# Kernel optimization log

Hardware: AMD Instinct MI355X
Metric: run time of the kernel (lower is better)

## Reference

```python
import jax, jax.numpy as jnp
import numpy as np

K = 16                 # k nearest neighbors
POS_LO, POS_HI = 0, 3  # position_slice
INF = jnp.float32(1e30)


def setup_inputs() -> dict:
    key = jax.random.key(0)
    k1, k2, k3 = jax.random.split(key, 3)
    B, N, F = 16, 2048, 128
    nodes = jax.random.normal(k1, (B, N, F), dtype=jnp.float32)
    T = jax.random.randint(k2, (B,), 0, 1024)
    taus = jax.random.randint(k3, (B,), 0, 1024)
    return {"nodes": nodes, "T": T, "taus": taus, "B": B}


def reference(nodes, T, taus, B):
    # Faithful, vectorized version of the per-batch causal KNN edge builder.
    # Original: for each batch b, sinks = pos[b, T[b]:T[b]+taus[b]],
    # sources = pos[b, :T[b]+taus[b]]; knn(source, sink, k) returns
    # (sink_local_idx, source_idx); keep edges where sink_local > source;
    # assemble COO adjacency (b, sink_local, source) with weight 1.
    # Here we return the equivalent DENSE [B, N, N] adjacency.
    pos = nodes[:, :, POS_LO:POS_HI]              # [B, N, d]
    N = pos.shape[1]
    i_idx = jnp.arange(N)                         # local sink index grid
    # global index of sink i in batch b is T[b] + i
    sink_gidx = jnp.clip(T[:, None] + i_idx[None, :], 0, N - 1)   # [B, N]
    sink_pos = jnp.take_along_axis(pos, sink_gidx[..., None], axis=1)  # [B, N, d]
    sink_valid = i_idx[None, :] < taus[:, None]                    # [B, N]
    src_valid = i_idx[None, :] < (T + taus)[:, None]               # [B, N]
    # squared distances sink->source: [B, N_sink, N_src]
    d2 = jnp.sum((sink_pos[:, :, None, :] - pos[:, None, :, :]) ** 2, axis=-1)
    d2 = jnp.where(src_valid[:, None, :], d2, INF)
    neg_vals, nbr = jax.lax.top_k(-d2, K)          # k smallest distances, [B, N, K]
    nbr_valid = neg_vals > -INF                    # source actually existed
    causal = i_idx[None, :, None] > nbr            # edge[0] > edge[1] mask (local sink idx)
    valid = sink_valid[:, :, None] & nbr_valid & causal
    adj = jnp.zeros((B, N, N), dtype=jnp.float32)
    b_idx = jnp.arange(B)[:, None, None]
    adj = adj.at[b_idx, i_idx[None, :, None], nbr].add(
        jnp.where(valid, jnp.float32(1.0), jnp.float32(0.0)))
    return adj
```

## Files before the change

kernel.cpp:

```cpp
#include <hip/hip_runtime.h>

#define NN 2048
#define FF 128
#define KK 16

__global__ __launch_bounds__(256) void knn_adj_kernel(
    const float* __restrict__ nodes,
    const int*   __restrict__ T_arr,
    const int*   __restrict__ tau_arr,
    float*       __restrict__ adj)
{
    const int b   = blockIdx.x;
    const int i0  = blockIdx.y << 2;
    const int tid = threadIdx.x;
    const int wave = tid >> 6;
    const int lane = tid & 63;

    const int T   = T_arr[b];
    const int tau = tau_arr[b];

    float* block_out = adj + ((size_t)b * NN + i0) * NN;

    if (i0 >= tau) {
        float4 z = make_float4(0.f, 0.f, 0.f, 0.f);
        float4* out4 = (float4*)block_out;
        #pragma unroll
        for (int t = 0; t < 8; ++t)
            out4[tid + (t << 8)] = z;
        return;
    }

    const int M = T + tau;

    __shared__ float sx[NN], sy[NN], sz[NN];
    for (int j = tid; j < M; j += 256) {
        const float* p = nodes + ((size_t)b * NN + j) * FF;
        sx[j] = p[0];
        sy[j] = p[1];
        sz[j] = p[2];
    }
    __syncthreads();

    const int i = i0 + wave;
    float* row_out = block_out + (size_t)wave * NN;

    if (i >= tau) {
        float4 z = make_float4(0.f, 0.f, 0.f, 0.f);
        float4* out4 = (float4*)row_out;
        #pragma unroll
        for (int t = 0; t < 8; ++t)
            out4[lane + (t << 6)] = z;
        return;
    }

    const int g = T + i;
    const float sxv = sx[g], syv = sy[g], szv = sz[g];

    unsigned long long keys[32];
    #pragma unroll
    for (int s = 0; s < 32; ++s) {
        const int j = lane + (s << 6);
        unsigned long long key = ~0ull;
        if (j < M) {
            float dx = __fsub_rn(sxv, sx[j]);
            float dy = __fsub_rn(syv, sy[j]);
            float dz = __fsub_rn(szv, sz[j]);
            float d2 = __fadd_rn(__fadd_rn(__fmul_rn(dx, dx), __fmul_rn(dy, dy)),
                                 __fmul_rn(dz, dz));
            key = ((unsigned long long)__float_as_uint(d2) << 32)
                | (unsigned int)(j + 1);
        }
        keys[s] = key;
    }

    const unsigned long long INF_HI = (unsigned long long)__float_as_uint(1e30f);

    unsigned int colmask = 0;
    unsigned long long prev = 0;
    for (int k = 0; k < KK; ++k) {
        unsigned long long m = ~0ull;
        #pragma unroll
        for (int s = 0; s < 32; ++s) {
            unsigned long long key = keys[s];
            if (key > prev && key < m) m = key;
        }
        #pragma unroll
        for (int off = 32; off > 0; off >>= 1) {
            unsigned long long o = __shfl_xor(m, off, 64);
            if (o < m) m = o;
        }
        if ((m >> 32) >= INF_HI) break;
        prev = m;
        const int j = (int)(m & 0xffffffffu) - 1;
        if (j < i && ((j >> 2) & 63) == lane)
            colmask |= 1u << (((j >> 8) << 2) | (j & 3));
    }

    float4* out4 = (float4*)row_out;
    #pragma unroll
    for (int t = 0; t < 8; ++t) {
        float4 v;
        v.x = ((colmask >> (t * 4 + 0)) & 1u) ? 1.0f : 0.0f;
        v.y = ((colmask >> (t * 4 + 1)) & 1u) ? 1.0f : 0.0f;
        v.z = ((colmask >> (t * 4 + 2)) & 1u) ? 1.0f : 0.0f;
        v.w = ((colmask >> (t * 4 + 3)) & 1u) ? 1.0f : 0.0f;
        out4[(t << 6) + lane] = v;
    }
}

extern "C" void kernel_launch(void* const* d_in, const int* in_sizes, int n_in,
                              void* d_out, int out_size, void* d_ws, size_t ws_size,
                              hipStream_t stream) {
    const float* nodes = (const float*)d_in[0];
    const int*   T     = (const int*)d_in[1];
    const int*   taus  = (const int*)d_in[2];
    float*       adj   = (float*)d_out;

    const int B = in_sizes[1];
    dim3 grid(B, NN / 4);
    knn_adj_kernel<<<grid, dim3(256), 0, stream>>>(nodes, T, taus, adj);
}
```

Baseline: 319.9 us.

## Split KNN into bitmap kernel with per-lane top-4 queue plus separate adjacency writer

The KNN is split into two kernels when workspace allows. The first keeps a per-lane sorted queue of the 4 smallest keys, picks the winner with a 32-bit DPP wave-min on the distance only, and rescans just when a lane's queue empties. It writes a compact per-row bitmap. The second kernel expands that bitmap into the dense float adjacency with coalesced float4 stores. This removes the 32-slot register key array and the 16 full scans per row, and stores positions as float4 in shared memory. In exchange it adds a second launch, a round trip through the workspace bitmap, and a data-dependent rescan path.

```diff
diff --git a/kernel.cpp b/kernel.cpp
--- a/kernel.cpp
+++ b/kernel.cpp
@@ -3,8 +3,158 @@
 #define NN 2048
 #define FF 128
 #define KK 16
-
-__global__ __launch_bounds__(256) void knn_adj_kernel(
+#define INF_KEY 0xFFFFFFFFFFFFFFFFull
+
+__device__ __forceinline__ unsigned long long make_key(const float4& s,
+                                                       const float4& p, int j) {
+    float dx = __fsub_rn(s.x, p.x);
+    float dy = __fsub_rn(s.y, p.y);
+    float dz = __fsub_rn(s.z, p.z);
+    float d2 = __fadd_rn(__fadd_rn(__fmul_rn(dx, dx), __fmul_rn(dy, dy)),
+                         __fmul_rn(dz, dz));
+    return ((unsigned long long)__float_as_uint(d2) << 32) | (unsigned)(j + 1);
+}
+
+__device__ __forceinline__ unsigned wave_min_u32(unsigned x) {
+    int v = (int)x, t;
+    t = __builtin_amdgcn_update_dpp(v, v, 0x111, 0xf, 0xf, false);
+    v = ((unsigned)t < (unsigned)v) ? t : v;
+    t = __builtin_amdgcn_update_dpp(v, v, 0x112, 0xf, 0xf, false);
+    v = ((unsigned)t < (unsigned)v) ? t : v;
+    t = __builtin_amdgcn_update_dpp(v, v, 0x114, 0xf, 0xf, false);
+    v = ((unsigned)t < (unsigned)v) ? t : v;
+    t = __builtin_amdgcn_update_dpp(v, v, 0x118, 0xf, 0xf, false);
+    v = ((unsigned)t < (unsigned)v) ? t : v;
+    t = __builtin_amdgcn_update_dpp(v, v, 0x142, 0xf, 0xf, false);
+    v = ((unsigned)t < (unsigned)v) ? t : v;
+    t = __builtin_amdgcn_update_dpp(v, v, 0x143, 0xf, 0xf, false);
+    v = ((unsigned)t < (unsigned)v) ? t : v;
+    return (unsigned)__builtin_amdgcn_readlane(v, 63);
+}
+
+__global__ __launch_bounds__(256) void knn_bitmap_kernel(
+    const float* __restrict__ nodes,
+    const int*   __restrict__ T_arr,
+    const int*   __restrict__ tau_arr,
+    unsigned*    __restrict__ bm)
+{
+    const int b    = blockIdx.x;
+    const int i0   = blockIdx.y << 2;
+    const int tid  = threadIdx.x;
+    const int wave = tid >> 6;
+    const int lane = tid & 63;
+
+    const int tau = tau_arr[b];
+    if (i0 >= tau) return;
+    const int T = T_arr[b];
+    const int M = T + tau;
+
+    __shared__ float4 spos[NN];
+    for (int j = tid; j < M; j += 256)
+        spos[j] = *(const float4*)(nodes + ((size_t)b * NN + j) * FF);
+    __syncthreads();
+
+    const int i = i0 + wave;
+    if (i >= tau) return;
+
+    const float4 sp = spos[T + i];
+
+    unsigned long long q0 = INF_KEY, q1 = INF_KEY, q2 = INF_KEY, q3 = INF_KEY;
+    const int S = (M + 63) >> 6;
+    #pragma unroll 4
+    for (int s = 0; s < S; ++s) {
+        const int j = lane + (s << 6);
+        if (j < M) {
+            unsigned long long key = make_key(sp, spos[j], j);
+            if (key < q3) {
+                q3 = key;
+                unsigned long long t;
+                if (q3 < q2) { t = q2; q2 = q3; q3 = t; }
+                if (q2 < q1) { t = q1; q1 = q2; q2 = t; }
+                if (q1 < q0) { t = q0; q0 = q1; q1 = t; }
+            }
+        }
+    }
+
+    unsigned colmask = 0;
+    unsigned long long lastpop = 0;
+    for (int k = 0; k < KK; ++k) {
+        const unsigned hd = (unsigned)(q0 >> 32);
+        const unsigned m  = wave_min_u32(hd);
+        if (m == 0xFFFFFFFFu) break;
+
+        const unsigned long long mask = __ballot(hd == m);
+        unsigned jwin;
+        if (__popcll(mask) == 1) {
+            const int w = __builtin_ctzll(mask);
+            jwin = (unsigned)__builtin_amdgcn_readlane((int)(unsigned)q0, w);
+        } else {
+            unsigned jc = (hd == m) ? (unsigned)q0 : 0xFFFFFFFFu;
+            jwin = wave_min_u32(jc);
+        }
+        const int j = (int)jwin - 1;
+
+        if (j < i && (j >> 5) == lane)
+            colmask |= 1u << (j & 31);
+
+        if (hd == m && (unsigned)q0 == jwin) {
+            lastpop = ((unsigned long long)m << 32) | jwin;
+            q0 = q1; q1 = q2; q2 = q3; q3 = INF_KEY;
+            if (q0 == INF_KEY) {
+                unsigned long long best = INF_KEY;
+                for (int s2 = 0; s2 < S; ++s2) {
+                    const int jj = lane + (s2 << 6);
+                    if (jj < M) {
+                        unsigned long long kk = make_key(sp, spos[jj], jj);
+                        if (kk > lastpop && kk < best) best = kk;
+                    }
+                }
+                q0 = best;
+            }
+        }
+    }
+
+    bm[((size_t)b * NN + i) * 64 + lane] = colmask;
+}
+
+__global__ __launch_bounds__(256) void write_adj_kernel(
+    const unsigned* __restrict__ bm,
+    const int*      __restrict__ tau_arr,
+    float*          __restrict__ adj)
+{
+    const int b    = blockIdx.x;
+    const int i0   = blockIdx.y << 2;
+    const int tid  = threadIdx.x;
+    const int wave = tid >> 6;
+    const int lane = tid & 63;
+    const int i    = i0 + wave;
+    const int tau  = tau_arr[b];
+
+    float4* out4 = (float4*)(adj + ((size_t)b * NN + i) * NN);
+
+    if (i >= tau) {
+        const float4 z = make_float4(0.f, 0.f, 0.f, 0.f);
+        #pragma unroll
+        for (int k = 0; k < 8; ++k)
+            out4[(k << 6) + lane] = z;
+        return;
+    }
+
+    const unsigned* row = bm + ((size_t)b * NN + i) * 64;
+    #pragma unroll
+    for (int k = 0; k < 8; ++k) {
+        const unsigned w   = row[(k << 3) + (lane >> 3)];
+        const unsigned nib = (w >> ((lane & 7) << 2)) & 0xFu;
+        float4 v;
+        v.x = (nib & 1u) ? 1.0f : 0.0f;
+        v.y = (nib & 2u) ? 1.0f : 0.0f;
+        v.z = (nib & 4u) ? 1.0f : 0.0f;
+        v.w = (nib & 8u) ? 1.0f : 0.0f;
+        out4[(k << 6) + lane] = v;
+    }
+}
+
+__global__ __launch_bounds__(256) void knn_adj_fused(
     const float* __restrict__ nodes,
     const int*   __restrict__ T_arr,
     const int*   __restrict__ tau_arr,
@@ -15,47 +165,35 @@
     const int tid = threadIdx.x;
     const int wave = tid >> 6;
     const int lane = tid & 63;
-
     const int T   = T_arr[b];
     const int tau = tau_arr[b];
-
     float* block_out = adj + ((size_t)b * NN + i0) * NN;
 
     if (i0 >= tau) {
         float4 z = make_float4(0.f, 0.f, 0.f, 0.f);
         float4* out4 = (float4*)block_out;
         #pragma unroll
-        for (int t = 0; t < 8; ++t)
-            out4[tid + (t << 8)] = z;
+        for (int t = 0; t < 8; ++t) out4[tid + (t << 8)] = z;
         return;
     }
-
     const int M = T + tau;
-
     __shared__ float sx[NN], sy[NN], sz[NN];
     for (int j = tid; j < M; j += 256) {
         const float* p = nodes + ((size_t)b * NN + j) * FF;
-        sx[j] = p[0];
-        sy[j] = p[1];
-        sz[j] = p[2];
+        sx[j] = p[0]; sy[j] = p[1]; sz[j] = p[2];
     }
     __syncthreads();
-
     const int i = i0 + wave;
     float* row_out = block_out + (size_t)wave * NN;
-
     if (i >= tau) {
         float4 z = make_float4(0.f, 0.f, 0.f, 0.f);
         float4* out4 = (float4*)row_out;
         #pragma unroll
-        for (int t = 0; t < 8; ++t)
-            out4[lane + (t << 6)] = z;
+        for (int t = 0; t < 8; ++t) out4[lane + (t << 6)] = z;
         return;
     }
-
     const int g = T + i;
     const float sxv = sx[g], syv = sy[g], szv = sz[g];
-
     unsigned long long keys[32];
     #pragma unroll
     for (int s = 0; s < 32; ++s) {
@@ -67,15 +205,12 @@
             float dz = __fsub_rn(szv, sz[j]);
             float d2 = __fadd_rn(__fadd_rn(__fmul_rn(dx, dx), __fmul_rn(dy, dy)),
                                  __fmul_rn(dz, dz));
-            key = ((unsigned long long)__float_as_uint(d2) << 32)
-                | (unsigned int)(j + 1);
+            key = ((unsigned long long)__float_as_uint(d2) << 32) | (unsigned)(j + 1);
         }
         keys[s] = key;
     }
-
     const unsigned long long INF_HI = (unsigned long long)__float_as_uint(1e30f);
-
-    unsigned int colmask = 0;
+    unsigned colmask = 0;
     unsigned long long prev = 0;
     for (int k = 0; k < KK; ++k) {
         unsigned long long m = ~0ull;
@@ -95,7 +230,6 @@
         if (j < i && ((j >> 2) & 63) == lane)
             colmask |= 1u << (((j >> 8) << 2) | (j & 3));
     }
-
     float4* out4 = (float4*)row_out;
     #pragma unroll
     for (int t = 0; t < 8; ++t) {
@@ -115,8 +249,16 @@
     const int*   T     = (const int*)d_in[1];
     const int*   taus  = (const int*)d_in[2];
     float*       adj   = (float*)d_out;
-
     const int B = in_sizes[1];
-    dim3 grid(B, NN / 4);
-    knn_adj_kernel<<<grid, dim3(256), 0, stream>>>(nodes, T, taus, adj);
-}
+
+    const size_t bm_bytes = (size_t)B * NN * 64 * sizeof(unsigned);
+    if (ws_size >= bm_bytes) {
+        unsigned* bm = (unsigned*)d_ws;
+        dim3 grid(B, NN / 4);
+        knn_bitmap_kernel<<<grid, dim3(256), 0, stream>>>(nodes, T, taus, bm);
+        write_adj_kernel<<<grid, dim3(256), 0, stream>>>(bm, taus, adj);
+    } else {
+        dim3 grid(B, NN / 4);
+        knn_adj_fused<<<grid, dim3(256), 0, stream>>>(nodes, T, taus, adj);
+    }
+}
```

Measured after the change: 316.1 us. Within noise of the previous version (-1.2%).

## Replace 16-pass full rescan with per-lane top-4 queues and DPP wave min

Applied to the files above, without the earlier changes.

Each lane now keeps a sorted queue of its 4 smallest keys instead of 32 keys in registers. Neighbours are popped with a 32-bit DPP wave minimum on the distance, and ties are broken by a second reduction on the index. A lane whose queue empties recomputes distances to refill it. The output bitmask is changed to contiguous 32-column words and redistributed through shared memory so the stores can be written as float4. The goal is to drop the per-iteration scan over 32 registers and the 64-bit shuffle reduction, and to lower register pressure. The cost is occasional refill rescans when one lane holds more than 4 of the winners.

```diff
diff --git a/kernel.cpp b/kernel.cpp
--- a/kernel.cpp
+++ b/kernel.cpp
@@ -3,26 +3,42 @@
 #define NN 2048
 #define FF 128
 #define KK 16
+#define INF_KEY 0xFFFFFFFFFFFFFFFFull
 
-__global__ __launch_bounds__(256) void knn_adj_kernel(
+__device__ __forceinline__ unsigned wave_min_u32(unsigned x) {
+    int v = (int)x, t;
+    t = __builtin_amdgcn_update_dpp(v, v, 0x111, 0xf, 0xf, false);
+    v = ((unsigned)t < (unsigned)v) ? t : v;
+    t = __builtin_amdgcn_update_dpp(v, v, 0x112, 0xf, 0xf, false);
+    v = ((unsigned)t < (unsigned)v) ? t : v;
+    t = __builtin_amdgcn_update_dpp(v, v, 0x114, 0xf, 0xf, false);
+    v = ((unsigned)t < (unsigned)v) ? t : v;
+    t = __builtin_amdgcn_update_dpp(v, v, 0x118, 0xf, 0xf, false);
+    v = ((unsigned)t < (unsigned)v) ? t : v;
+    t = __builtin_amdgcn_update_dpp(v, v, 0x142, 0xf, 0xf, false);
+    v = ((unsigned)t < (unsigned)v) ? t : v;
+    t = __builtin_amdgcn_update_dpp(v, v, 0x143, 0xf, 0xf, false);
+    v = ((unsigned)t < (unsigned)v) ? t : v;
+    return (unsigned)__builtin_amdgcn_readlane(v, 63);
+}
+
+__global__ __launch_bounds__(256) void knn_adj_fused(
     const float* __restrict__ nodes,
     const int*   __restrict__ T_arr,
     const int*   __restrict__ tau_arr,
     float*       __restrict__ adj)
 {
-    const int b   = blockIdx.x;
-    const int i0  = blockIdx.y << 2;
-    const int tid = threadIdx.x;
+    const int b    = blockIdx.x;
+    const int i0   = blockIdx.y << 2;
+    const int tid  = threadIdx.x;
     const int wave = tid >> 6;
     const int lane = tid & 63;
 
-    const int T   = T_arr[b];
     const int tau = tau_arr[b];
-
     float* block_out = adj + ((size_t)b * NN + i0) * NN;
 
     if (i0 >= tau) {
-        float4 z = make_float4(0.f, 0.f, 0.f, 0.f);
+        const float4 z = make_float4(0.f, 0.f, 0.f, 0.f);
         float4* out4 = (float4*)block_out;
         #pragma unroll
         for (int t = 0; t < 8; ++t)
@@ -30,9 +46,11 @@
         return;
     }
 
+    const int T = T_arr[b];
     const int M = T + tau;
 
     __shared__ float sx[NN], sy[NN], sz[NN];
+    __shared__ unsigned swords[4][64];
     for (int j = tid; j < M; j += 256) {
         const float* p = nodes + ((size_t)b * NN + j) * FF;
         sx[j] = p[0];
@@ -42,69 +60,99 @@
     __syncthreads();
 
     const int i = i0 + wave;
-    float* row_out = block_out + (size_t)wave * NN;
+    float4* out4 = (float4*)(block_out + (size_t)wave * NN);
 
     if (i >= tau) {
-        float4 z = make_float4(0.f, 0.f, 0.f, 0.f);
-        float4* out4 = (float4*)row_out;
+        const float4 z = make_float4(0.f, 0.f, 0.f, 0.f);
         #pragma unroll
         for (int t = 0; t < 8; ++t)
-            out4[lane + (t << 6)] = z;
+            out4[(t << 6) + lane] = z;
         return;
     }
 
     const int g = T + i;
     const float sxv = sx[g], syv = sy[g], szv = sz[g];
 
-    unsigned long long keys[32];
-    #pragma unroll
-    for (int s = 0; s < 32; ++s) {
+    unsigned long long q0 = INF_KEY, q1 = INF_KEY, q2 = INF_KEY, q3 = INF_KEY;
+    const int S = (M + 63) >> 6;
+    #pragma unroll 4
+    for (int s = 0; s < S; ++s) {
         const int j = lane + (s << 6);
-        unsigned long long key = ~0ull;
         if (j < M) {
             float dx = __fsub_rn(sxv, sx[j]);
             float dy = __fsub_rn(syv, sy[j]);
             float dz = __fsub_rn(szv, sz[j]);
             float d2 = __fadd_rn(__fadd_rn(__fmul_rn(dx, dx), __fmul_rn(dy, dy)),
                                  __fmul_rn(dz, dz));
-            key = ((unsigned long long)__float_as_uint(d2) << 32)
-                | (unsigned int)(j + 1);
+            unsigned long long key =
+                ((unsigned long long)__float_as_uint(d2) << 32) | (unsigned)(j + 1);
+            if (key < q3) {
+                q3 = key;
+                unsigned long long t;
+                if (q3 < q2) { t = q2; q2 = q3; q3 = t; }
+                if (q2 < q1) { t = q1; q1 = q2; q2 = t; }
+                if (q1 < q0) { t = q0; q0 = q1; q1 = t; }
+            }
         }
-        keys[s] = key;
     }
 
-    const unsigned long long INF_HI = (unsigned long long)__float_as_uint(1e30f);
+    unsigned colmask = 0;
+    unsigned long long lastpop = 0;
+    for (int k = 0; k < KK; ++k) {
+        const unsigned hd = (unsigned)(q0 >> 32);
+        const unsigned m  = wave_min_u32(hd);
+        if (m == 0xFFFFFFFFu) break;
 
-    unsigned int colmask = 0;
-    unsigned long long prev = 0;
-    for (int k = 0; k < KK; ++k) {
-        unsigned long long m = ~0ull;
-        #pragma unroll
-        for (int s = 0; s < 32; ++s) {
-            unsigned long long key = keys[s];
-            if (key > prev && key < m) m = key;
+        const unsigned long long mask = __ballot(hd == m);
+        unsigned jwin;
+        if (__popcll(mask) == 1) {
+            const int w = __builtin_ctzll(mask);
+            jwin = (unsigned)__builtin_amdgcn_readlane((int)(unsigned)q0, w);
+        } else {
+            unsigned jc = (hd == m) ? (unsigned)q0 : 0xFFFFFFFFu;
+            jwin = wave_min_u32(jc);
         }
-        #pragma unroll
-        for (int off = 32; off > 0; off >>= 1) {
-            unsigned long long o = __shfl_xor(m, off, 64);
-            if (o < m) m = o;
+        const int j = (int)jwin - 1;
+
+        if (j < i && (j >> 5) == lane)
+            colmask |= 1u << (j & 31);
+
+        if (hd == m && (unsigned)q0 == jwin) {
+            lastpop = ((unsigned long long)m << 32) | jwin;
+            q0 = q1; q1 = q2; q2 = q3; q3 = INF_KEY;
+            if (q0 == INF_KEY) {
+                unsigned long long best = INF_KEY;
+                for (int s2 = 0; s2 < S; ++s2) {
+                    const int jj = lane + (s2 << 6);
+                    if (jj < M) {
+                        float dx = __fsub_rn(sxv, sx[jj]);
+                        float dy = __fsub_rn(syv, sy[jj]);
+                        float dz = __fsub_rn(szv, sz[jj]);
+                        float d2 = __fadd_rn(
+                            __fadd_rn(__fmul_rn(dx, dx), __fmul_rn(dy, dy)),
+                            __fmul_rn(dz, dz));
+                        unsigned long long kk =
+                            ((unsigned long long)__float_as_uint(d2) << 32)
+                            | (unsigned)(jj + 1);
+                        if (kk > lastpop && kk < best) best = kk;
+                    }
+                }
+                q0 = best;
+            }
         }
-        if ((m >> 32) >= INF_HI) break;
-        prev = m;
-        const int j = (int)(m & 0xffffffffu) - 1;
-        if (j < i && ((j >> 2) & 63) == lane)
-            colmask |= 1u << (((j >> 8) << 2) | (j & 3));
     }
 
-    float4* out4 = (float4*)row_out;
+    swords[wave][lane] = colmask;
     #pragma unroll
-    for (int t = 0; t < 8; ++t) {
+    for (int k = 0; k < 8; ++k) {
+        const unsigned w   = swords[wave][(k << 3) + (lane >> 3)];
+        const unsigned nib = (w >> ((lane & 7) << 2)) & 0xFu;
         float4 v;
-        v.x = ((colmask >> (t * 4 + 0)) & 1u) ? 1.0f : 0.0f;
-        v.y = ((colmask >> (t * 4 + 1)) & 1u) ? 1.0f : 0.0f;
-        v.z = ((colmask >> (t * 4 + 2)) & 1u) ? 1.0f : 0.0f;
-        v.w = ((colmask >> (t * 4 + 3)) & 1u) ? 1.0f : 0.0f;
-        out4[(t << 6) + lane] = v;
+        v.x = (nib & 1u) ? 1.0f : 0.0f;
+        v.y = (nib & 2u) ? 1.0f : 0.0f;
+        v.z = (nib & 4u) ? 1.0f : 0.0f;
+        v.w = (nib & 8u) ? 1.0f : 0.0f;
+        out4[(k << 6) + lane] = v;
     }
 }
 
@@ -115,8 +163,8 @@
     const int*   T     = (const int*)d_in[1];
     const int*   taus  = (const int*)d_in[2];
     float*       adj   = (float*)d_out;
+    const int B = in_sizes[1];
 
-    const int B = in_sizes[1];
     dim3 grid(B, NN / 4);
-    knn_adj_kernel<<<grid, dim3(256), 0, stream>>>(nodes, T, taus, adj);
+    knn_adj_fused<<<grid, dim3(256), 0, stream>>>(nodes, T, taus, adj);
 }
```

Measured after the change: 276.3 us. 13.6% less time.
